# Optimization experiments

Measured on AMD Instinct MI355X. Metric: run time of the kernel, lower is better.

The kernel has to match this reference:

```python
import jax, jax.numpy as jnp
import numpy as np

N_HEADS = 8
HEAD_DIM = 48  # d_model 384 / 8 heads
D_MODEL = 384


def setup_inputs() -> dict:
    key = jax.random.key(0)
    k1, k2, k3, k4, k5 = jax.random.split(key, 5)
    B, S = 8, 2048
    return {
        "x": jax.random.normal(k1, (B, S, D_MODEL), dtype=jnp.float32),
        "W_qkv": jax.random.normal(k2, (3 * D_MODEL, D_MODEL), dtype=jnp.float32) * 0.02,
        "b_qkv": jax.random.normal(k3, (3 * D_MODEL,), dtype=jnp.float32) * 0.02,
        "W_o": jax.random.normal(k4, (D_MODEL, D_MODEL), dtype=jnp.float32) * 0.02,
        "b_o": jax.random.normal(k5, (D_MODEL,), dtype=jnp.float32) * 0.02,
    }


def reference(x, W_qkv, b_qkv, W_o, b_o):
    B, S, D = x.shape
    H, hd = N_HEADS, HEAD_DIM
    # fused QKV projection: [B,S,3D]
    qkv = jnp.einsum("bsd,ed->bse", x, W_qkv) + b_qkv
    # [B,S,H,3*hd] -> [B,H,S,3*hd]
    qkv = qkv.reshape(B, S, H, 3 * hd).transpose(0, 2, 1, 3)
    Q, K, V = jnp.split(qkv, 3, axis=-1)  # each [B,H,S,hd]
    scale = 1.0 / np.sqrt(hd).astype(np.float32)
    scores = jnp.einsum("bhqd,bhkd->bhqk", Q, K) * scale  # [B,H,S,S]
    # NOTE: original softmaxes over dim=1 (heads), not the key dim
    attn = jax.nn.softmax(scores, axis=1)
    values = jnp.einsum("bhqk,bhkd->bhqd", attn, V)  # [B,H,S,hd]
    # NOTE: original reshapes [B,H,S,hd] directly to [B,S,H*hd] (no permute back)
    values = values.reshape(B, S, H * hd)
    out = jnp.einsum("bsd,ed->bse", values, W_o) + b_o
    return out
```

## Files before the change

### kernel.cpp

```cpp
#include <hip/hip_runtime.h>
#include <hip/hip_bf16.h>

#define BB 8
#define SS 2048
#define DD 384
#define HH 8
#define HD 48
#define QT 32
#define KT 32

typedef unsigned short u16;
typedef unsigned int u32;
typedef unsigned short u16x4 __attribute__((ext_vector_type(4)));
typedef unsigned short u16x8 __attribute__((ext_vector_type(8)));
typedef unsigned int u32x2 __attribute__((ext_vector_type(2)));
typedef short s16x8 __attribute__((ext_vector_type(8)));
typedef float f32x4 __attribute__((ext_vector_type(4)));

__device__ __forceinline__ float bf2f(u16 v){
  union { u32 u; float f; } x; x.u = ((u32)v) << 16; return x.f;
}
__device__ __forceinline__ u16 f2bf(float f){
  union { float f; u32 u; } x; x.f = f;
  u32 r = x.u + 0x7fffu + ((x.u >> 16) & 1u);
  return (u16)(r >> 16);
}
__device__ __forceinline__ void split2(float f, u16& h, u16& l){
  union { float f; u32 u; } x; x.f = f;
  h = (u16)(x.u >> 16);
  l = f2bf(f - bf2f(h));
}
__device__ __forceinline__ u32 pack_trunc2(float a, float b){
  union { float f; u32 u; } xa, xb; xa.f = a; xb.f = b;
  return (xa.u >> 16) | (xb.u & 0xffff0000u);
}

#define LBAR() do { \
  asm volatile("s_waitcnt lgkmcnt(0)" ::: "memory"); \
  __builtin_amdgcn_s_barrier(); \
  asm volatile("" ::: "memory"); \
} while (0)

__global__ __launch_bounds__(512, 4) void qkv_gemm(
    const float* __restrict__ x, const float* __restrict__ W,
    const float* __restrict__ bias,
    u16* __restrict__ Q, u16* __restrict__ Kd, u16* __restrict__ Vt)
{
  __shared__ u16 Ah[128][40], Al[128][40], Bh[128][40], Bl[128][40];
  const int tid  = threadIdx.x;
  const int w    = tid >> 6, lane = tid & 63;
  const int lg   = lane >> 4, ln = lane & 15;
  const int wm   = w >> 1, wn = w & 1;
  const int mb   = blockIdx.x / 9, nb = blockIdx.x % 9;
  const int m0   = mb * 128, n0 = nb * 128;
  const int srow = tid >> 3, sk4 = (tid & 7) << 2;
  const float qscale = 0.2082350972f;

  f32x4 acc[8];
  #pragma unroll
  for (int i = 0; i < 8; i++) acc[i] = (f32x4){0.f,0.f,0.f,0.f};

  for (int ks = 0; ks < 12; ks++){
    const int k0 = ks * 32;
    __syncthreads();
    #pragma unroll
    for (int p = 0; p < 2; p++){
      const int row = srow + p*64;
      float4 av = *(const float4*)(x + (long)(m0+row)*DD + k0 + sk4);
      float4 bv = *(const float4*)(W + (long)(n0+row)*DD + k0 + sk4);
      u16 h0,l0,h1,l1,h2,l2,h3,l3;
      split2(av.x,h0,l0); split2(av.y,h1,l1); split2(av.z,h2,l2); split2(av.w,h3,l3);
      *(u16x4*)&Ah[row][sk4] = (u16x4){h0,h1,h2,h3};
      *(u16x4*)&Al[row][sk4] = (u16x4){l0,l1,l2,l3};
      split2(bv.x,h0,l0); split2(bv.y,h1,l1); split2(bv.z,h2,l2); split2(bv.w,h3,l3);
      *(u16x4*)&Bh[row][sk4] = (u16x4){h0,h1,h2,h3};
      *(u16x4*)&Bl[row][sk4] = (u16x4){l0,l1,l2,l3};
    }
    __syncthreads();
    s16x8 bh[4], bl[4];
    #pragma unroll
    for (int fn = 0; fn < 4; fn++){
      const int br = wn*64 + fn*16 + ln;
      bh[fn] = *(const s16x8*)&Bh[br][lg*8];
      bl[fn] = *(const s16x8*)&Bl[br][lg*8];
    }
    #pragma unroll
    for (int fm = 0; fm < 2; fm++){
      const int ar = wm*32 + fm*16 + ln;
      s16x8 ah = *(const s16x8*)&Ah[ar][lg*8];
      s16x8 al = *(const s16x8*)&Al[ar][lg*8];
      #pragma unroll
      for (int fn = 0; fn < 4; fn++){
        f32x4 c = acc[fm*4+fn];
        c = __builtin_amdgcn_mfma_f32_16x16x32_bf16(ah, bh[fn], c, 0, 0, 0);
        c = __builtin_amdgcn_mfma_f32_16x16x32_bf16(ah, bl[fn], c, 0, 0, 0);
        c = __builtin_amdgcn_mfma_f32_16x16x32_bf16(al, bh[fn], c, 0, 0, 0);
        acc[fm*4+fn] = c;
      }
    }
  }
  #pragma unroll
  for (int fm = 0; fm < 2; fm++){
    #pragma unroll
    for (int fn = 0; fn < 4; fn++){
      const int e = n0 + wn*64 + fn*16 + ln;
      const float bi = bias[e];
      const int h = e / 144, c = e % 144;
      #pragma unroll
      for (int r = 0; r < 4; r++){
        const int mm = m0 + wm*32 + fm*16 + lg*4 + r;
        const int bb = mm >> 11, s = mm & 2047;
        const float v = acc[fm*4+fn][r] + bi;
        if (c < 48){
          Q[(((long)(bb*HH + h))*SS + s)*HD + c] = f2bf(v * qscale);
        } else if (c < 96){
          Kd[(((long)(bb*HH + h))*SS + s)*HD + (c-48)] = f2bf(v);
        } else {
          Vt[(((long)(bb*HH + h))*HD + (c-96))*SS + s] = f2bf(v);
        }
      }
    }
  }
}

__global__ __launch_bounds__(512, 4) void attn_kernel(
    const u16* __restrict__ Q, const u16* __restrict__ K,
    const u16* __restrict__ Vg, float* __restrict__ vals)
{
  __shared__ u16 Ss[HH][QT][40];
  __shared__ u16 Pb[HH][QT][40];

  const int tid  = threadIdx.x;
  const int h    = tid >> 6;
  const int lane = tid & 63;
  const int wg   = ((int)blockIdx.x % 8) * 64 + (int)blockIdx.x / 8;
  const int b    = wg >> 6;
  const int qt   = wg & 63;
  const int q0   = qt * QT;
  const int lg   = lane >> 4;
  const int ln   = lane & 15;

  const long hbase = ((long)(b*HH + h)) * SS;
  const u16* vbase = Vg + ((long)(b*HH + h)) * HD * SS;
  const s16x8 z8 = (s16x8){0,0,0,0,0,0,0,0};

  s16x8 qf0[2], qf1[2];
  #pragma unroll
  for (int qs = 0; qs < 2; qs++){
    const u16* qp = Q + (hbase + q0 + qs*16 + ln)*HD;
    qf0[qs] = *(const s16x8*)(qp + lg*8);
    if (lane < 32) qf1[qs] = *(const s16x8*)(qp + 32 + lg*8);
    else           qf1[qs] = z8;
  }

  f32x4 oacc[2][3];
  #pragma unroll
  for (int qs = 0; qs < 2; qs++)
    #pragma unroll
    for (int c = 0; c < 3; c++) oacc[qs][c] = (f32x4){0.f,0.f,0.f,0.f};

  const int smq = tid >> 4, smk = (tid & 15) << 1;

  s16x8 kfA[2][2], kfB[2][2];
  int k0 = 0;
  #pragma unroll
  for (int nt = 0; nt < 2; nt++){
    const u16* kp = K + (hbase + nt*16 + ln)*HD;
    kfA[0][nt] = *(const s16x8*)(kp + lg*8);
    if (lane < 32) kfB[0][nt] = *(const s16x8*)(kp + 32 + lg*8);
    else           kfB[0][nt] = z8;
  }

#define STEP(CUR, NXT) { \
     \
    s16x8 vf0 = *(const s16x8*)(vbase + (long)(     ln)*SS + k0 + lg*8); \
    s16x8 vf1 = *(const s16x8*)(vbase + (long)(16 + ln)*SS + k0 + lg*8); \
    s16x8 vf2 = *(const s16x8*)(vbase + (long)(32 + ln)*SS + k0 + lg*8); \
     \
    const int knx = (k0 + KT) & (SS - 1); \
    _Pragma("unroll") \
    for (int nt = 0; nt < 2; nt++){ \
      const u16* kp = K + (hbase + knx + nt*16 + ln)*HD; \
      kfA[NXT][nt] = *(const s16x8*)(kp + lg*8); \
      if (lane < 32) kfB[NXT][nt] = *(const s16x8*)(kp + 32 + lg*8); \
      else           kfB[NXT][nt] = z8; \
    } \
     \
    __builtin_amdgcn_s_setprio(1); \
    _Pragma("unroll") \
    for (int nt = 0; nt < 2; nt++){ \
      _Pragma("unroll") \
      for (int qs = 0; qs < 2; qs++){ \
        f32x4 a = (f32x4){0.f,0.f,0.f,0.f}; \
        a = __builtin_amdgcn_mfma_f32_16x16x32_bf16(kfA[CUR][nt], qf0[qs], a, 0, 0, 0); \
        a = __builtin_amdgcn_mfma_f32_16x16x32_bf16(kfB[CUR][nt], qf1[qs], a, 0, 0, 0); \
        u32x2 pw; pw[0] = pack_trunc2(a[0], a[1]); pw[1] = pack_trunc2(a[2], a[3]); \
        *(u32x2*)&Ss[h][qs*16 + ln][nt*16 + lg*4] = pw; \
      } \
    } \
    __builtin_amdgcn_s_setprio(0); \
    LBAR();    \
     \
    { \
      float e0[8], e1[8]; \
      float sum0 = 0.f, sum1 = 0.f; \
      _Pragma("unroll") \
      for (int hh = 0; hh < 8; hh++){ \
        u32 wv = *(const u32*)&Ss[hh][smq][smk]; \
        union { u32 u; float f; } a0, a1; \
        a0.u = wv << 16; a1.u = wv & 0xffff0000u; \
        e0[hh] = __builtin_amdgcn_exp2f(a0.f); \
        e1[hh] = __builtin_amdgcn_exp2f(a1.f); \
        sum0 += e0[hh]; sum1 += e1[hh]; \
      } \
      float r0 = __builtin_amdgcn_rcpf(sum0); \
      float r1 = __builtin_amdgcn_rcpf(sum1); \
      _Pragma("unroll") \
      for (int hh = 0; hh < 8; hh++) \
        *(u32*)&Pb[hh][smq][smk] = pack_trunc2(e0[hh]*r0, e1[hh]*r1); \
    } \
    LBAR();    \
    __builtin_amdgcn_s_setprio(1); \
    _Pragma("unroll") \
    for (int qs = 0; qs < 2; qs++){ \
      s16x8 pf = *(const s16x8*)&Pb[h][qs*16 + ln][lg*8]; \
      oacc[qs][0] = __builtin_amdgcn_mfma_f32_16x16x32_bf16(pf, vf0, oacc[qs][0], 0, 0, 0); \
      oacc[qs][1] = __builtin_amdgcn_mfma_f32_16x16x32_bf16(pf, vf1, oacc[qs][1], 0, 0, 0); \
      oacc[qs][2] = __builtin_amdgcn_mfma_f32_16x16x32_bf16(pf, vf2, oacc[qs][2], 0, 0, 0); \
    } \
    __builtin_amdgcn_s_setprio(0); \
    k0 = knx; \
  }

  for (int kt2 = 0; kt2 < SS/KT/2; kt2++){
    STEP(0, 1)
    STEP(1, 0)
  }
#undef STEP

  float* op = vals + (hbase + q0)*HD;
  #pragma unroll
  for (int qs = 0; qs < 2; qs++)
    #pragma unroll
    for (int c = 0; c < 3; c++)
      #pragma unroll
      for (int r = 0; r < 4; r++)
        op[(long)(qs*16 + lg*4 + r)*HD + c*16 + ln] = oacc[qs][c][r];
}

__global__ __launch_bounds__(512, 4) void out_gemm(
    const float* __restrict__ A, const float* __restrict__ W,
    const float* __restrict__ bias, float* __restrict__ out)
{
  __shared__ u16 Ah[128][40], Al[128][40], Bh[128][40], Bl[128][40];
  const int tid  = threadIdx.x;
  const int w    = tid >> 6, lane = tid & 63;
  const int lg   = lane >> 4, ln = lane & 15;
  const int wm   = w >> 1, wn = w & 1;
  const int mb   = blockIdx.x / 3, nb = blockIdx.x % 3;
  const int m0   = mb * 128, n0 = nb * 128;
  const int srow = tid >> 3, sk4 = (tid & 7) << 2;

  f32x4 acc[8];
  #pragma unroll
  for (int i = 0; i < 8; i++) acc[i] = (f32x4){0.f,0.f,0.f,0.f};

  for (int ks = 0; ks < 12; ks++){
    const int k0 = ks * 32;
    __syncthreads();
    #pragma unroll
    for (int p = 0; p < 2; p++){
      const int row = srow + p*64;
      float4 av = *(const float4*)(A + (long)(m0+row)*DD + k0 + sk4);
      float4 bv = *(const float4*)(W + (long)(n0+row)*DD + k0 + sk4);
      u16 h0,l0,h1,l1,h2,l2,h3,l3;
      split2(av.x,h0,l0); split2(av.y,h1,l1); split2(av.z,h2,l2); split2(av.w,h3,l3);
      *(u16x4*)&Ah[row][sk4] = (u16x4){h0,h1,h2,h3};
      *(u16x4*)&Al[row][sk4] = (u16x4){l0,l1,l2,l3};
      split2(bv.x,h0,l0); split2(bv.y,h1,l1); split2(bv.z,h2,l2); split2(bv.w,h3,l3);
      *(u16x4*)&Bh[row][sk4] = (u16x4){h0,h1,h2,h3};
      *(u16x4*)&Bl[row][sk4] = (u16x4){l0,l1,l2,l3};
    }
    __syncthreads();
    s16x8 bh[4], bl[4];
    #pragma unroll
    for (int fn = 0; fn < 4; fn++){
      const int br = wn*64 + fn*16 + ln;
      bh[fn] = *(const s16x8*)&Bh[br][lg*8];
      bl[fn] = *(const s16x8*)&Bl[br][lg*8];
    }
    #pragma unroll
    for (int fm = 0; fm < 2; fm++){
      const int ar = wm*32 + fm*16 + ln;
      s16x8 ah = *(const s16x8*)&Ah[ar][lg*8];
      s16x8 al = *(const s16x8*)&Al[ar][lg*8];
      #pragma unroll
      for (int fn = 0; fn < 4; fn++){
        f32x4 c = acc[fm*4+fn];
        c = __builtin_amdgcn_mfma_f32_16x16x32_bf16(ah, bh[fn], c, 0, 0, 0);
        c = __builtin_amdgcn_mfma_f32_16x16x32_bf16(ah, bl[fn], c, 0, 0, 0);
        c = __builtin_amdgcn_mfma_f32_16x16x32_bf16(al, bh[fn], c, 0, 0, 0);
        acc[fm*4+fn] = c;
      }
    }
  }
  #pragma unroll
  for (int fm = 0; fm < 2; fm++){
    #pragma unroll
    for (int fn = 0; fn < 4; fn++){
      const int e = n0 + wn*64 + fn*16 + ln;
      const float bi = bias[e];
      #pragma unroll
      for (int r = 0; r < 4; r++){
        const int mm = m0 + wm*32 + fm*16 + lg*4 + r;
        out[(long)mm*DD + e] = acc[fm*4+fn][r] + bi;
      }
    }
  }
}

extern "C" void kernel_launch(void* const* d_in, const int* in_sizes, int n_in,
                              void* d_out, int out_size, void* d_ws, size_t ws_size,
                              hipStream_t stream)
{
  const float* x    = (const float*)d_in[0];
  const float* Wqkv = (const float*)d_in[1];
  const float* bqkv = (const float*)d_in[2];
  const float* Wo   = (const float*)d_in[3];
  const float* bo   = (const float*)d_in[4];
  float* out = (float*)d_out;

  const size_t QSZ = (size_t)BB*HH*SS*HD;
  u16* Q  = (u16*)d_ws;
  u16* K  = Q + QSZ;
  u16* Vt = K + QSZ;
  float* vals = (float*)(Vt + QSZ);

  qkv_gemm<<<1152, 512, 0, stream>>>(x, Wqkv, bqkv, Q, K, Vt);
  attn_kernel<<<512, 512, 0, stream>>>(Q, K, Vt, vals);
  out_gemm<<<384, 512, 0, stream>>>(vals, Wo, bo, out);
}
```

Before: 224.0 us.

## Split attention key range across two workgroups and sum partials in output GEMM

The attention kernel gains a key-split parameter, so each workgroup handles half the keys for a query tile. The grid doubles to 1024 blocks, giving more parallelism than 512 blocks offer on the device. The partial outputs go to two separate buffers and are summed in the output GEMM's A-load. This works because the softmax runs over heads rather than keys, so contributions from different keys add linearly. The cost is double the fp32 intermediate traffic, and the split path depends on the workspace being large enough.

New measurement: 238.5 us. +6.5%, slower.

```diff
diff --git a/kernel.cpp b/kernel.cpp
--- a/kernel.cpp
+++ b/kernel.cpp
@@ -125,7 +125,7 @@
 
 __global__ __launch_bounds__(512, 4) void attn_kernel(
     const u16* __restrict__ Q, const u16* __restrict__ K,
-    const u16* __restrict__ Vg, float* __restrict__ vals)
+    const u16* __restrict__ Vg, float* __restrict__ vals, const int ks_bits)
 {
   __shared__ u16 Ss[HH][QT][40];
   __shared__ u16 Pb[HH][QT][40];
@@ -133,9 +133,12 @@
   const int tid  = threadIdx.x;
   const int h    = tid >> 6;
   const int lane = tid & 63;
-  const int wg   = ((int)blockIdx.x % 8) * 64 + (int)blockIdx.x / 8;
-  const int b    = wg >> 6;
-  const int qt   = wg & 63;
+  const int b    = (int)blockIdx.x & 7;
+  const int rem  = (int)blockIdx.x >> 3;
+  const int qt   = rem >> ks_bits;
+  const int ks   = rem & ((1 << ks_bits) - 1);
+  const int koff = ks << (11 - ks_bits);
+  const int nit2 = 32 >> ks_bits;
   const int q0   = qt * QT;
   const int lg   = lane >> 4;
   const int ln   = lane & 15;
@@ -162,10 +165,10 @@
   const int smq = tid >> 4, smk = (tid & 15) << 1;
 
   s16x8 kfA[2][2], kfB[2][2];
-  int k0 = 0;
+  int k0 = koff;
   #pragma unroll
   for (int nt = 0; nt < 2; nt++){
-    const u16* kp = K + (hbase + nt*16 + ln)*HD;
+    const u16* kp = K + (hbase + koff + nt*16 + ln)*HD;
     kfA[0][nt] = *(const s16x8*)(kp + lg*8);
     if (lane < 32) kfB[0][nt] = *(const s16x8*)(kp + 32 + lg*8);
     else           kfB[0][nt] = z8;
@@ -232,13 +235,13 @@
     k0 = knx; \
   }
 
-  for (int kt2 = 0; kt2 < SS/KT/2; kt2++){
+  for (int kt2 = 0; kt2 < nit2; kt2++){
     STEP(0, 1)
     STEP(1, 0)
   }
 #undef STEP
 
-  float* op = vals + (hbase + q0)*HD;
+  float* op = vals + (size_t)ks * ((size_t)BB*HH*SS*HD) + (hbase + q0)*HD;
   #pragma unroll
   for (int qs = 0; qs < 2; qs++)
     #pragma unroll
@@ -249,7 +252,8 @@
 }
 
 __global__ __launch_bounds__(512, 4) void out_gemm(
-    const float* __restrict__ A, const float* __restrict__ W,
+    const float* __restrict__ A, const float* __restrict__ A2,
+    const float* __restrict__ W,
     const float* __restrict__ bias, float* __restrict__ out)
 {
   __shared__ u16 Ah[128][40], Al[128][40], Bh[128][40], Bl[128][40];
@@ -271,7 +275,12 @@
     #pragma unroll
     for (int p = 0; p < 2; p++){
       const int row = srow + p*64;
-      float4 av = *(const float4*)(A + (long)(m0+row)*DD + k0 + sk4);
+      const long aoff = (long)(m0+row)*DD + k0 + sk4;
+      float4 av = *(const float4*)(A + aoff);
+      if (A2){
+        float4 a2 = *(const float4*)(A2 + aoff);
+        av.x += a2.x; av.y += a2.y; av.z += a2.z; av.w += a2.w;
+      }
       float4 bv = *(const float4*)(W + (long)(n0+row)*DD + k0 + sk4);
       u16 h0,l0,h1,l1,h2,l2,h3,l3;
       split2(av.x,h0,l0); split2(av.y,h1,l1); split2(av.z,h2,l2); split2(av.w,h3,l3);
@@ -336,7 +345,14 @@
   u16* Vt = K + QSZ;
   float* vals = (float*)(Vt + QSZ);
 
+  const size_t need2 = 3*QSZ*sizeof(u16) + 2*QSZ*sizeof(float);
+
   qkv_gemm<<<1152, 512, 0, stream>>>(x, Wqkv, bqkv, Q, K, Vt);
-  attn_kernel<<<512, 512, 0, stream>>>(Q, K, Vt, vals);
-  out_gemm<<<384, 512, 0, stream>>>(vals, Wo, bo, out);
-}
+  if (ws_size >= need2){
+    attn_kernel<<<1024, 512, 0, stream>>>(Q, K, Vt, vals, 1);
+    out_gemm<<<384, 512, 0, stream>>>(vals, vals + QSZ, Wo, bo, out);
+  } else {
+    attn_kernel<<<512, 512, 0, stream>>>(Q, K, Vt, vals, 0);
+    out_gemm<<<384, 512, 0, stream>>>(vals, nullptr, Wo, bo, out);
+  }
+}
```
